# Performance work log

Measured on AMD Instinct MI355X. Metric: run time of the kernel, lower is better.

Reference implementation:

```python
import jax, jax.numpy as jnp
import numpy as np

EMB_LEN = 1024
HEAD_SIZE = 64

def setup_inputs() -> dict:
    key = jax.random.key(0)
    k1, k2, k3, k4 = jax.random.split(key, 4)
    input_emb = jax.random.normal(k1, (8, 4096, EMB_LEN), dtype=jnp.float32)
    # nn.Linear weights are [out, in]; applied as x @ W.T
    Wq = jax.random.normal(k2, (HEAD_SIZE, EMB_LEN), dtype=jnp.float32) * (EMB_LEN ** -0.5)
    Wk = jax.random.normal(k3, (HEAD_SIZE, EMB_LEN), dtype=jnp.float32) * (EMB_LEN ** -0.5)
    Wv = jax.random.normal(k4, (HEAD_SIZE, EMB_LEN), dtype=jnp.float32) * (EMB_LEN ** -0.5)
    return {"input_emb": input_emb, "Wq": Wq, "Wk": Wk, "Wv": Wv}

def reference(input_emb, Wq, Wk, Wv):
    B, S, E = input_emb.shape
    scale = jnp.asarray(HEAD_SIZE, input_emb.dtype) ** -0.5
    q = jnp.einsum('bse,he->bsh', input_emb, Wq)  # [B,S,H]
    k = jnp.einsum('bse,he->bsh', input_emb, Wk)
    v = jnp.einsum('bse,he->bsh', input_emb, Wv)
    scores = jnp.einsum('bqh,bkh->bqk', q, k) * scale  # [B,S,S]
    causal = jnp.tril(jnp.ones((S, S), dtype=bool))
    scores = jnp.where(causal, scores, -jnp.inf)
    attn = jax.nn.softmax(scores, axis=-1)
    return jnp.einsum('bqk,bkh->bqh', attn, v)
```

## Files before the change

kernel.cpp:

```cpp
#include <hip/hip_runtime.h>
#include <hip/hip_bf16.h>

#define EMB 1024
#define HS 64
#define SEQ 4096

using bf16x8 = __attribute__((ext_vector_type(8))) __bf16;
using f32x4  = __attribute__((ext_vector_type(4))) float;

__device__ __forceinline__ ushort f2b(float f) {
    unsigned x = __float_as_uint(f);
    return (ushort)((x + 0x7fffu + ((x >> 16) & 1u)) >> 16);
}

__global__ void cvt_w(const float* __restrict__ wq, const float* __restrict__ wk,
                      const float* __restrict__ wv, ushort* __restrict__ wcat) {
    int i = blockIdx.x * 256 + threadIdx.x;
    const int n = HS * EMB;
    if (i >= 3 * n) return;
    float f;
    if (i < n)          f = wq[i];
    else if (i < 2 * n) f = wk[i - n];
    else                f = wv[i - 2 * n];
    wcat[i] = f2b(f);
}

__global__ __launch_bounds__(1024) void qkv_proj(
        const float* __restrict__ x, const ushort* __restrict__ wcat,
        ushort* __restrict__ qo, ushort* __restrict__ ko, ushort* __restrict__ vo) {
    __shared__ ushort Xs[64][72];
    __shared__ ushort Ws[192][72];
    const int t = threadIdx.x;
    const int lane = t & 63, wid = t >> 6;
    const int g = lane >> 4, c = lane & 15;
    const int strip = wid >> 2, colq = wid & 3;
    const int row0 = blockIdx.x * 64;

    f32x4 acc[3];
#pragma unroll
    for (int i = 0; i < 3; ++i) acc[i] = f32x4{0.f, 0.f, 0.f, 0.f};

    for (int kc = 0; kc < EMB; kc += 64) {
        __syncthreads();
        {
            int e = t * 4, r = e >> 6, cc = e & 63;
            float4 v = *reinterpret_cast<const float4*>(&x[(row0 + r) * EMB + kc + cc]);
            ushort4 u;
            u.x = f2b(v.x); u.y = f2b(v.y); u.z = f2b(v.z); u.w = f2b(v.w);
            *reinterpret_cast<ushort4*>(&Xs[r][cc]) = u;
        }
#pragma unroll
        for (int i = 0; i < 3; ++i) {
            int e = (i * 1024 + t) * 4, r = e >> 6, cc = e & 63;
            *reinterpret_cast<ushort4*>(&Ws[r][cc]) =
                *reinterpret_cast<const ushort4*>(&wcat[r * EMB + kc + cc]);
        }
        __syncthreads();
#pragma unroll
        for (int kk = 0; kk < 2; ++kk) {
            bf16x8 a = *reinterpret_cast<const bf16x8*>(&Xs[strip * 16 + c][kk * 32 + 8 * g]);
#pragma unroll
            for (int nt = 0; nt < 3; ++nt) {
                bf16x8 b = *reinterpret_cast<const bf16x8*>(
                    &Ws[(colq * 3 + nt) * 16 + c][kk * 32 + 8 * g]);
                acc[nt] = __builtin_amdgcn_mfma_f32_16x16x32_bf16(a, b, acc[nt], 0, 0, 0);
            }
        }
    }

    const float qs = 0.125f * 1.44269504f;
#pragma unroll
    for (int nt = 0; nt < 3; ++nt) {
        int col = (colq * 3 + nt) * 16 + c;
        int rowb = row0 + strip * 16 + 4 * g;
        if (col < 64) {
#pragma unroll
            for (int r = 0; r < 4; ++r)
                qo[(rowb + r) * 64 + col] = f2b(acc[nt][r] * qs);
        } else if (col < 128) {
#pragma unroll
            for (int r = 0; r < 4; ++r)
                ko[(rowb + r) * 64 + (col - 64)] = f2b(acc[nt][r]);
        } else {
            int b = rowb >> 12, s0 = rowb & 4095;
            ushort4 pv;
            pv.x = f2b(acc[nt][0]); pv.y = f2b(acc[nt][1]);
            pv.z = f2b(acc[nt][2]); pv.w = f2b(acc[nt][3]);
            *reinterpret_cast<ushort4*>(&vo[(b * 64 + (col - 128)) * SEQ + s0]) = pv;
        }
    }
}

__global__ __launch_bounds__(256) void attn(
        const ushort* __restrict__ q, const ushort* __restrict__ k,
        const ushort* __restrict__ vt, float* __restrict__ out) {
    __shared__ __align__(16) char smem[40960];

    const int t = threadIdx.x;
    const int lane = t & 63, w = t >> 6;
    const int g = lane >> 4, c = lane & 15;
    const int sp = w & 1, pp = w >> 1;

    const int bid = blockIdx.x;
    const int batch = bid & 7;
    const int qt = 63 - (bid >> 3);
    const int q0b = qt * 64;
    const int npairs = qt + 1;

    const char* kbч = (const char*)(k + (size_t)batch * SEQ * 64);
    const char* vbч = (const char*)(vt + (size_t)batch * 64 * SEQ);
    const ushort* qb = q + (size_t)batch * SEQ * 64;

    auto stage_pair = [&](int cpair) {
#pragma unroll
        for (int n = 0; n < 4; ++n) {
            int idx = w * 4 + n;
            int cpar = idx >> 3, rest = idx & 7, isV = rest >> 2, f = rest & 3;
            int kv0 = (cpair * 2 + cpar) * 32;
            const char* src;
            if (!isV)
                src = kbч + (size_t)(kv0 + (f >> 1) * 16 + c) * 128 + (f & 1) * 64 + 16 * g;
            else
                src = vbч + (size_t)(f * 16 + c) * (SEQ * 2) + kv0 * 2 + 16 * g;
            char* dst = smem + (cpair & 1) * 16384 + cpar * 8192 + isV * 4096 + f * 1024;
            __builtin_amdgcn_global_load_lds(
                (const __attribute__((address_space(1))) void*)src,
                (__attribute__((address_space(3))) void*)dst, 16, 0, 0);
        }
    };

    bf16x8 qa[2][2];
#pragma unroll
    for (int ss = 0; ss < 2; ++ss)
#pragma unroll
        for (int kk = 0; kk < 2; ++kk)
            qa[ss][kk] = *reinterpret_cast<const bf16x8*>(
                &qb[(q0b + sp * 32 + ss * 16 + c) * 64 + kk * 32 + 8 * g]);

    f32x4 accO[2][4];
#pragma unroll
    for (int ss = 0; ss < 2; ++ss)
#pragma unroll
        for (int nt = 0; nt < 4; ++nt) accO[ss][nt] = f32x4{0.f, 0.f, 0.f, 0.f};
    float lsum[2][4] = {{0.f, 0.f, 0.f, 0.f}, {0.f, 0.f, 0.f, 0.f}};

    stage_pair(0);
    asm volatile("s_waitcnt vmcnt(0)" ::: "memory");
    __syncthreads();

    const int pbase = 32768 + w * 2048 + (((c >> 3) * 16 + 4 * g) * 16) + (c & 7) * 2;

    for (int cpair = 0; cpair < npairs; ++cpair) {
        if (cpair + 1 < npairs) stage_pair(cpair + 1);

        const char* tb = smem + (cpair & 1) * 16384 + pp * 8192;

        f32x4 sA[2][2];
#pragma unroll
        for (int ss = 0; ss < 2; ++ss)
#pragma unroll
            for (int kt = 0; kt < 2; ++kt) sA[ss][kt] = f32x4{0.f, 0.f, 0.f, 0.f};
#pragma unroll
        for (int kk = 0; kk < 2; ++kk)
#pragma unroll
            for (int kt = 0; kt < 2; ++kt) {
                bf16x8 kf = *reinterpret_cast<const bf16x8*>(tb + (kt * 2 + kk) * 1024 + lane * 16);
                sA[0][kt] = __builtin_amdgcn_mfma_f32_16x16x32_bf16(qa[0][kk], kf, sA[0][kt], 0, 0, 0);
                sA[1][kt] = __builtin_amdgcn_mfma_f32_16x16x32_bf16(qa[1][kk], kf, sA[1][kt], 0, 0, 0);
            }

        if (cpair == npairs - 1) {
#pragma unroll
            for (int ss = 0; ss < 2; ++ss)
#pragma unroll
                for (int kt = 0; kt < 2; ++kt) {
                    int kvl = pp * 32 + kt * 16 + c;
#pragma unroll
                    for (int r = 0; r < 4; ++r) {
                        int ql = sp * 32 + ss * 16 + 4 * g + r;
                        if (kvl > ql) sA[ss][kt][r] = -INFINITY;
                    }
                }
        }

#pragma unroll
        for (int ss = 0; ss < 2; ++ss)
#pragma unroll
            for (int kt = 0; kt < 2; ++kt)
#pragma unroll
                for (int r = 0; r < 4; ++r) {
                    float p = __builtin_amdgcn_exp2f(sA[ss][kt][r]);
                    lsum[ss][r] += p;
                    *(ushort*)(smem + pbase + ss * 1024 + kt * 512 + r * 16) = f2b(p);
                }

        bf16x8 pa0 = *reinterpret_cast<const bf16x8*>(smem + 32768 + w * 2048 + lane * 16);
        bf16x8 pa1 = *reinterpret_cast<const bf16x8*>(smem + 32768 + w * 2048 + 1024 + lane * 16);

#pragma unroll
        for (int nt = 0; nt < 4; ++nt) {
            bf16x8 vf = *reinterpret_cast<const bf16x8*>(tb + 4096 + nt * 1024 + lane * 16);
            accO[0][nt] = __builtin_amdgcn_mfma_f32_16x16x32_bf16(pa0, vf, accO[0][nt], 0, 0, 0);
            accO[1][nt] = __builtin_amdgcn_mfma_f32_16x16x32_bf16(pa1, vf, accO[1][nt], 0, 0, 0);
        }

        asm volatile("s_waitcnt vmcnt(0)" ::: "memory");
        __syncthreads();
    }

#pragma unroll
    for (int off = 1; off < 16; off <<= 1)
#pragma unroll
        for (int ss = 0; ss < 2; ++ss)
#pragma unroll
            for (int r = 0; r < 4; ++r)
                lsum[ss][r] += __shfl_xor(lsum[ss][r], off, 64);

    if (pp == 1) {
#pragma unroll
        for (int ss = 0; ss < 2; ++ss)
#pragma unroll
            for (int nt = 0; nt < 4; ++nt)
#pragma unroll
                for (int r = 0; r < 4; ++r)
                    *(float*)(smem + sp * 8192 + (ss * 16 + 4 * g + r) * 256 + (nt * 16 + c) * 4) =
                        accO[ss][nt][r];
        if (c == 0)
#pragma unroll
            for (int ss = 0; ss < 2; ++ss)
#pragma unroll
                for (int r = 0; r < 4; ++r)
                    *(float*)(smem + 16384 + sp * 128 + (ss * 16 + 4 * g + r) * 4) = lsum[ss][r];
    }
    __syncthreads();
    if (pp == 0) {
        float* ob = out + (size_t)batch * SEQ * 64;
#pragma unroll
        for (int ss = 0; ss < 2; ++ss)
#pragma unroll
            for (int nt = 0; nt < 4; ++nt)
#pragma unroll
                for (int r = 0; r < 4; ++r) {
                    float a2 = *(float*)(smem + sp * 8192 + (ss * 16 + 4 * g + r) * 256 + (nt * 16 + c) * 4);
                    float l2 = *(float*)(smem + 16384 + sp * 128 + (ss * 16 + 4 * g + r) * 4);
                    ob[(q0b + sp * 32 + ss * 16 + 4 * g + r) * 64 + nt * 16 + c] =
                        (accO[ss][nt][r] + a2) / (lsum[ss][r] + l2);
                }
    }
}

extern "C" void kernel_launch(void* const* d_in, const int* in_sizes, int n_in,
                              void* d_out, int out_size, void* d_ws, size_t ws_size,
                              hipStream_t stream) {
    const float* x  = (const float*)d_in[0];
    const float* wq = (const float*)d_in[1];
    const float* wk = (const float*)d_in[2];
    const float* wv = (const float*)d_in[3];
    float* out = (float*)d_out;

    char* ws = (char*)d_ws;
    ushort* wcat = (ushort*)ws;
    ushort* qo   = (ushort*)(ws + 393216);
    ushort* ko   = (ushort*)(ws + 393216 + 4194304);
    ushort* vo   = (ushort*)(ws + 393216 + 2 * 4194304);

    hipLaunchKernelGGL(cvt_w, dim3(768), dim3(256), 0, stream, wq, wk, wv, wcat);
    hipLaunchKernelGGL(qkv_proj, dim3(512), dim3(1024), 0, stream, x, wcat, qo, ko, vo);
    hipLaunchKernelGGL(attn, dim3(512), dim3(256), 0, stream, qo, ko, vo, out);
}
```

Before: 96.78 us.

## Triple-buffer K/V staging with one barrier per iteration

Replaces the double-buffered K/V tile staging with a three-slot ring. Loads now run two tiles ahead, and each iteration waits only for the older tile's loads (vmcnt(4)) before a single barrier, instead of a full drain plus barrier at the end of every iteration. This is meant to hide global-to-LDS latency and remove one synchronisation per step. In exchange LDS use grows from 40 KB to 56 KB per block, which may reduce how many blocks fit on a CU, and the partial vmcnt wait relies on each thread issuing exactly four loads per stage.

```diff
diff --git a/kernel.cpp b/kernel.cpp
--- a/kernel.cpp
+++ b/kernel.cpp
@@ -94,7 +94,7 @@
 __global__ __launch_bounds__(256) void attn(
         const ushort* __restrict__ q, const ushort* __restrict__ k,
         const ushort* __restrict__ vt, float* __restrict__ out) {
-    __shared__ __align__(16) char smem[40960];
+    __shared__ __align__(16) char smem[57344];
 
     const int t = threadIdx.x;
     const int lane = t & 63, w = t >> 6;
@@ -107,11 +107,11 @@
     const int q0b = qt * 64;
     const int npairs = qt + 1;
 
-    const char* kbч = (const char*)(k + (size_t)batch * SEQ * 64);
-    const char* vbч = (const char*)(vt + (size_t)batch * 64 * SEQ);
+    const char* kbp = (const char*)(k + (size_t)batch * SEQ * 64);
+    const char* vbp = (const char*)(vt + (size_t)batch * 64 * SEQ);
     const ushort* qb = q + (size_t)batch * SEQ * 64;
 
-    auto stage_pair = [&](int cpair) {
+    auto stage_pair = [&](int cpair, char* base) {
 #pragma unroll
         for (int n = 0; n < 4; ++n) {
             int idx = w * 4 + n;
@@ -119,10 +119,10 @@
             int kv0 = (cpair * 2 + cpar) * 32;
             const char* src;
             if (!isV)
-                src = kbч + (size_t)(kv0 + (f >> 1) * 16 + c) * 128 + (f & 1) * 64 + 16 * g;
+                src = kbp + (size_t)(kv0 + (f >> 1) * 16 + c) * 128 + (f & 1) * 64 + 16 * g;
             else
-                src = vbч + (size_t)(f * 16 + c) * (SEQ * 2) + kv0 * 2 + 16 * g;
-            char* dst = smem + (cpair & 1) * 16384 + cpar * 8192 + isV * 4096 + f * 1024;
+                src = vbp + (size_t)(f * 16 + c) * (SEQ * 2) + kv0 * 2 + 16 * g;
+            char* dst = base + cpar * 8192 + isV * 4096 + f * 1024;
             __builtin_amdgcn_global_load_lds(
                 (const __attribute__((address_space(1))) void*)src,
                 (__attribute__((address_space(3))) void*)dst, 16, 0, 0);
@@ -144,16 +144,24 @@
         for (int nt = 0; nt < 4; ++nt) accO[ss][nt] = f32x4{0.f, 0.f, 0.f, 0.f};
     float lsum[2][4] = {{0.f, 0.f, 0.f, 0.f}, {0.f, 0.f, 0.f, 0.f}};
 
-    stage_pair(0);
-    asm volatile("s_waitcnt vmcnt(0)" ::: "memory");
-    __syncthreads();
-
-    const int pbase = 32768 + w * 2048 + (((c >> 3) * 16 + 4 * g) * 16) + (c & 7) * 2;
+    stage_pair(0, smem);
+    if (npairs > 1) stage_pair(1, smem + 16384);
+
+    const int pbase = 49152 + w * 2048 + (((c >> 3) * 16 + 4 * g) * 16) + (c & 7) * 2;
+    int bcur = 0;
 
     for (int cpair = 0; cpair < npairs; ++cpair) {
-        if (cpair + 1 < npairs) stage_pair(cpair + 1);
-
-        const char* tb = smem + (cpair & 1) * 16384 + pp * 8192;
+        if (cpair + 1 < npairs) asm volatile("s_waitcnt vmcnt(4)" ::: "memory");
+        else                    asm volatile("s_waitcnt vmcnt(0)" ::: "memory");
+        __builtin_amdgcn_s_barrier();
+        __builtin_amdgcn_sched_barrier(0);
+
+        if (cpair + 2 < npairs) {
+            int bn = bcur + 2; if (bn >= 3) bn -= 3;
+            stage_pair(cpair + 2, smem + bn * 16384);
+        }
+
+        const char* tb = smem + bcur * 16384 + pp * 8192;
 
         f32x4 sA[2][2];
 #pragma unroll
@@ -194,8 +202,8 @@
                     *(ushort*)(smem + pbase + ss * 1024 + kt * 512 + r * 16) = f2b(p);
                 }
 
-        bf16x8 pa0 = *reinterpret_cast<const bf16x8*>(smem + 32768 + w * 2048 + lane * 16);
-        bf16x8 pa1 = *reinterpret_cast<const bf16x8*>(smem + 32768 + w * 2048 + 1024 + lane * 16);
+        bf16x8 pa0 = *reinterpret_cast<const bf16x8*>(smem + 49152 + w * 2048 + lane * 16);
+        bf16x8 pa1 = *reinterpret_cast<const bf16x8*>(smem + 49152 + w * 2048 + 1024 + lane * 16);
 
 #pragma unroll
         for (int nt = 0; nt < 4; ++nt) {
@@ -204,8 +212,7 @@
             accO[1][nt] = __builtin_amdgcn_mfma_f32_16x16x32_bf16(pa1, vf, accO[1][nt], 0, 0, 0);
         }
 
-        asm volatile("s_waitcnt vmcnt(0)" ::: "memory");
-        __syncthreads();
+        bcur = (bcur + 1 == 3) ? 0 : bcur + 1;
     }
 
 #pragma unroll
@@ -216,6 +223,7 @@
             for (int r = 0; r < 4; ++r)
                 lsum[ss][r] += __shfl_xor(lsum[ss][r], off, 64);
 
+    __syncthreads();
     if (pp == 1) {
 #pragma unroll
         for (int ss = 0; ss < 2; ++ss)
```

Result: no change. 95.91 us (-0.9%).
